# Kernel optimization log

Hardware: AMD Instinct MI355X
Metric: run time of the kernel (lower is better)

Reference implementation:

```python
import jax, jax.numpy as jnp
import numpy as np

DIM = 512
HEADS = 8
DIM_HEAD = 64
HIDDEN = HEADS * DIM_HEAD  # 512
B, H, W = 32, 64, 64


def setup_inputs() -> dict:
    key = jax.random.key(0)
    k1, k2, k3 = jax.random.split(key, 3)
    x = jax.random.normal(k1, (B, H, W, DIM), dtype=jnp.float32)
    w_qkv = jax.random.normal(k2, (DIM, 3 * HIDDEN), dtype=jnp.float32) * 0.02
    w_out = jax.random.normal(k3, (HIDDEN, DIM), dtype=jnp.float32) * 0.02
    b_out = jnp.zeros((DIM,), dtype=jnp.float32)
    return {"x": x, "w_qkv": w_qkv, "w_out": w_out, "b_out": b_out}


def reference(x, w_qkv, w_out, b_out):
    b, h, w, c = x.shape
    n = h * w
    scale = DIM_HEAD ** (-0.5)
    # 1x1 conv (no bias) == matmul over channels
    qkv = jnp.einsum('bhwc,cf->bhwf', x, w_qkv)  # (b, h, w, 3*hidden)
    q, k, v = jnp.split(qkv, 3, axis=-1)
    # 'b x y (h c) -> b (x y) h c'
    def to_heads(t):
        return t.reshape(b, n, HEADS, DIM_HEAD)
    q, k, v = map(to_heads, (q, k, v))
    q = q * scale
    # contraction over spatial axis d=(x*y): sim (b, dim_head_i, heads, dim_head_j)
    sim = jnp.einsum('bdhi,bdhj->bihj', q, k)
    sim = sim - jnp.max(sim, axis=-1, keepdims=True)
    attn = jax.nn.softmax(sim, axis=-1)
    out = jnp.einsum('bihj,bdhj->bdhi', attn, v)  # (b, n, heads, dim_head)
    out = out.reshape(b, h, w, HIDDEN)
    # output 1x1 conv with bias
    return jnp.einsum('bhwf,fc->bhwc', out, w_out) + b_out
```

## Files before the change

### kernel.cpp

```cpp
#include <hip/hip_runtime.h>
#include <hip/hip_bf16.h>
#include <stdint.h>

using bf16x8 = __attribute__((ext_vector_type(8))) __bf16;
using s16x8  = __attribute__((ext_vector_type(8))) short;
using f32x4  = __attribute__((ext_vector_type(4))) float;

__device__ __forceinline__ uint16_t f2bf(float f) {
    uint32_t u = __builtin_bit_cast(uint32_t, f);
    u += 0x7fffu + ((u >> 16) & 1u);
    return (uint16_t)(u >> 16);
}
__device__ __forceinline__ float bf2f(uint16_t h) {
    return __builtin_bit_cast(float, (uint32_t)h << 16);
}

__device__ __forceinline__ void async16(uint16_t* lds_dst, const uint16_t* g_src) {
    __builtin_amdgcn_global_load_lds(
        (const __attribute__((address_space(1))) void*)g_src,
        (__attribute__((address_space(3))) void*)lds_dst,
        16, 0, 0);
}

__global__ void wprep_all(const float* __restrict__ wqkv, const float* __restrict__ wout,
                          uint16_t* __restrict__ wqTs, uint16_t* __restrict__ wkTcat,
                          uint16_t* __restrict__ woutT, uint16_t* __restrict__ wv_rm)
{
    int sec = blockIdx.x >> 10;
    int idx = (blockIdx.x & 1023) * 256 + threadIdx.x;
    int co = idx >> 9, r = idx & 511;
    if (sec == 0) {
        wqTs[co * 512 + r] = f2bf(wqkv[r * 1536 + co] * 0.125f);
    } else if (sec == 1) {
        uint16_t v = f2bf(wqkv[r * 1536 + 512 + co]);
        wkTcat[co * 1024 + r] = v;
        wkTcat[co * 1024 + 512 + r] = v;
    } else if (sec == 2) {
        woutT[co * 512 + r] = f2bf(wout[r * 512 + co]);
    } else {
        wv_rm[co * 512 + r] = f2bf(wqkv[co * 1536 + 1024 + r]);
    }
}

__global__ __launch_bounds__(256, 4)
void xt_k(const float* __restrict__ x, uint16_t* __restrict__ xb, uint16_t* __restrict__ xT)
{
    __shared__ uint16_t lt[64 * 68];
    const int tid = threadIdx.x;
    const int bi = blockIdx.x;
    const int b = bi >> 9;
    const int rem = bi & 511;
    const int st = rem >> 3, ct = rem & 7;
    const int c4 = (tid & 15) * 4;
#pragma unroll
    for (int rep = 0; rep < 4; ++rep) {
        int r = (tid >> 4) + rep * 16;
        long gs = (long)(b * 4096 + st * 64 + r) * 512 + ct * 64 + c4;
        float4 v = *(const float4*)(x + gs);
        uint16_t t[4];
        t[0] = f2bf(v.x); t[1] = f2bf(v.y); t[2] = f2bf(v.z); t[3] = f2bf(v.w);
        *(ushort4*)(xb + gs) = *(const ushort4*)t;
#pragma unroll
        for (int q = 0; q < 4; ++q) lt[r * 68 + c4 + q] = t[q];
    }
    __syncthreads();
    const int s4 = (tid & 15) * 4;
#pragma unroll
    for (int rep = 0; rep < 4; ++rep) {
        int c = (tid >> 4) + rep * 16;
        uint16_t t[4];
#pragma unroll
        for (int q = 0; q < 4; ++q) t[q] = lt[(s4 + q) * 68 + c];
        *(ushort4*)(xT + (long)(b * 512 + ct * 64 + c) * 4096 + st * 64 + s4) =
            *(const ushort4*)t;
    }
}

template<bool OUTF32>
__global__ __launch_bounds__(512, 2)
void g8_k(const uint16_t* __restrict__ A, const uint16_t* __restrict__ Bt,
          void* __restrict__ Cp, const float* __restrict__ bias,
          int K, int lda, int ldb, int ldc, int mtiles, int ntiles,
          long abr, long bbe, long cbr)
{
    __shared__ uint16_t lds[65536];
    const int tid  = threadIdx.x;
    const int lane = tid & 63;
    const int wv   = tid >> 6;
    const int wr   = wv >> 2, wc = wv & 3;

    const int q8 = gridDim.x >> 3;
    const int l  = (blockIdx.x & 7) * q8 + (blockIdx.x >> 3);
    const int per   = mtiles * ntiles;
    const int batch = l / per;
    const int rem   = l - batch * per;
    const int mt    = rem / ntiles, nt = rem - mt * ntiles;

    const long arow0 = abr * batch + (long)mt * 256;
    const uint16_t* abase = A + arow0 * (long)lda;
    const uint16_t* btb   = Bt + bbe * batch + (long)nt * 256 * ldb;

    const int fr = lane & 15;
    const int cx0 = (((0 << 2) | (lane >> 4)) ^ (fr & 7)) * 8;
    const int cx1 = (((1 << 2) | (lane >> 4)) ^ (fr & 7)) * 8;
    const int baseA = wr * 8192 + fr * 64;
    const int baseB = (2 + (wc >> 1)) * 8192 + ((wc & 1) * 64 + fr) * 64;

    const int NT = K >> 6;

    auto stage = [&](int slot, const uint16_t* gb, int rstride, int k0) {
#pragma unroll
        for (int i = 0; i < 2; ++i) {
            int si = i * 512 + wv * 64 + lane;
            int rr = si >> 3, cc = (si & 7) ^ (rr & 7);
            async16(&lds[slot * 8192 + (i * 512 + wv * 64) * 8],
                    gb + (long)rr * rstride + k0 + cc * 8);
        }
    };

    f32x4 acc[8][4];
#pragma unroll
    for (int m = 0; m < 8; ++m)
#pragma unroll
        for (int n = 0; n < 4; ++n) acc[m][n] = (f32x4){0.f, 0.f, 0.f, 0.f};

    bf16x8 af[4], bfq[4];

    auto rdA = [&](int mb, int b4, int cx) {
#pragma unroll
        for (int mi = 0; mi < 4; ++mi)
            af[mi] = __builtin_bit_cast(bf16x8,
                *(const s16x8*)&lds[b4 * 8192 + baseA + (mb + mi) * 1024 + cx]);
    };
    auto rdB = [&](int b4, int cx) {
#pragma unroll
        for (int n = 0; n < 4; ++n)
            bfq[n] = __builtin_bit_cast(bf16x8,
                *(const s16x8*)&lds[b4 * 8192 + baseB + n * 1024 + cx]);
    };
    auto mm = [&](int mb) {
        asm volatile("s_waitcnt lgkmcnt(0)" ::: "memory");
        __builtin_amdgcn_sched_barrier(0);
        __builtin_amdgcn_s_setprio(1);
#pragma unroll
        for (int mi = 0; mi < 4; ++mi)
#pragma unroll
            for (int n = 0; n < 4; ++n)
                acc[mb + mi][n] = __builtin_amdgcn_mfma_f32_16x16x32_bf16(
                    af[mi], bfq[n], acc[mb + mi][n], 0, 0, 0);
        __builtin_amdgcn_s_setprio(0);
        __builtin_amdgcn_s_barrier();
    };

    stage(0, abase,              lda, 0);
    stage(1, abase + 128L * lda, lda, 0);
    stage(2, btb,                ldb, 0);
    stage(3, btb + 128L * ldb,   ldb, 0);
    stage(6, btb,                ldb, 64);
    stage(7, btb + 128L * ldb,   ldb, 64);
    asm volatile("s_waitcnt vmcnt(4)" ::: "memory");
    __builtin_amdgcn_sched_barrier(0);
    __builtin_amdgcn_s_barrier();

    for (int it = 0; it < (NT >> 1); ++it) {
        const int E = 2 * it, Od = E + 1;
        const bool s3 = (E + 2) < NT;
        const bool s7 = (Od + 2) < NT;
        const int kE2 = (E + 2) << 6, kO1 = Od << 6, kO2 = (Od + 2) << 6;

        rdB(0, cx0); rdA(0, 0, cx0);
        stage(4, abase,              lda, kO1);
        stage(5, abase + 128L * lda, lda, kO1);
        __builtin_amdgcn_s_barrier();
        mm(0);
        rdA(4, 0, cx0);
        __builtin_amdgcn_s_barrier();
        mm(4);
        rdB(0, cx1); rdA(0, 0, cx1);
        __builtin_amdgcn_s_barrier();
        mm(0);
        rdA(4, 0, cx1);
        if (s3) {
            stage(2, btb,              ldb, kE2);
            stage(3, btb + 128L * ldb, ldb, kE2);
            asm volatile("s_waitcnt vmcnt(4)" ::: "memory");
        } else {
            asm volatile("s_waitcnt vmcnt(0)" ::: "memory");
        }
        __builtin_amdgcn_sched_barrier(0);
        __builtin_amdgcn_s_barrier();
        mm(4);
        rdB(4, cx0); rdA(0, 4, cx0);
        if (s3) {
            stage(0, abase,              lda, kE2);
            stage(1, abase + 128L * lda, lda, kE2);
        }
        __builtin_amdgcn_s_barrier();
        mm(0);
        rdA(4, 4, cx0);
        __builtin_amdgcn_s_barrier();
        mm(4);
        rdB(4, cx1); rdA(0, 4, cx1);
        __builtin_amdgcn_s_barrier();
        mm(0);
        rdA(4, 4, cx1);
        if (s7) {
            stage(6, btb,              ldb, kO2);
            stage(7, btb + 128L * ldb, ldb, kO2);
            asm volatile("s_waitcnt vmcnt(4)" ::: "memory");
        } else {
            asm volatile("s_waitcnt vmcnt(0)" ::: "memory");
        }
        __builtin_amdgcn_sched_barrier(0);
        __builtin_amdgcn_s_barrier();
        mm(4);
    }

    const long crow0 = cbr * batch + (long)mt * 256 + wr * 128;
    const int  col0  = nt * 256 + wc * 64;
    float bv[4];
#pragma unroll
    for (int n = 0; n < 4; ++n)
        bv[n] = bias ? bias[col0 + n * 16 + (lane & 15)] : 0.f;
#pragma unroll
    for (int m = 0; m < 8; ++m) {
#pragma unroll
        for (int r = 0; r < 4; ++r) {
            long row = crow0 + m * 16 + (lane >> 4) * 4 + r;
#pragma unroll
            for (int n = 0; n < 4; ++n) {
                int col = col0 + n * 16 + (lane & 15);
                float v = acc[m][n][r];
                if constexpr (OUTF32)
                    ((float*)Cp)[row * (long)ldc + col] = v + bv[n];
                else
                    ((uint16_t*)Cp)[row * (long)ldc + col] = f2bf(v);
            }
        }
    }
}

__global__ __launch_bounds__(512, 2)
void g8G_k(const uint16_t* __restrict__ X, uint16_t* __restrict__ Gcat)
{
    __shared__ uint16_t lds[65536];
    const int tid  = threadIdx.x;
    const int lane = tid & 63;
    const int wv   = tid >> 6;
    const int wr   = wv >> 2, wc = wv & 3;

    const int q8 = gridDim.x >> 3;
    const int l  = (blockIdx.x & 7) * q8 + (blockIdx.x >> 3);
    const int g  = l / 3;
    const int quad = l - g * 3;
    const int b = g >> 1, z = g & 1;
    const int mt = (quad == 1) ? 1 : 0;
    const int nt = (quad == 0) ? 0 : 1;

    const uint16_t* xb0 = X + (long)b * 512 * 4096 + z * 2048;
    const uint16_t* abase = xb0 + (long)mt * 256 * 4096;
    const uint16_t* btb   = xb0 + (long)nt * 256 * 4096;

    const int fr = lane & 15;
    const int cx0 = (((0 << 2) | (lane >> 4)) ^ (fr & 7)) * 8;
    const int cx1 = (((1 << 2) | (lane >> 4)) ^ (fr & 7)) * 8;
    const int baseA = wr * 8192 + fr * 64;
    const int baseB = (2 + (wc >> 1)) * 8192 + ((wc & 1) * 64 + fr) * 64;

    const int NT = 32;

    auto stage = [&](int slot, const uint16_t* gb, int k0) {
#pragma unroll
        for (int i = 0; i < 2; ++i) {
            int si = i * 512 + wv * 64 + lane;
            int rr = si >> 3, cc = (si & 7) ^ (rr & 7);
            async16(&lds[slot * 8192 + (i * 512 + wv * 64) * 8],
                    gb + (long)rr * 4096 + k0 + cc * 8);
        }
    };

    f32x4 acc[8][4];
#pragma unroll
    for (int m = 0; m < 8; ++m)
#pragma unroll
        for (int n = 0; n < 4; ++n) acc[m][n] = (f32x4){0.f, 0.f, 0.f, 0.f};

    bf16x8 af[4], bfq[4];
    auto rdA = [&](int mb, int b4, int cx) {
#pragma unroll
        for (int mi = 0; mi < 4; ++mi)
            af[mi] = __builtin_bit_cast(bf16x8,
                *(const s16x8*)&lds[b4 * 8192 + baseA + (mb + mi) * 1024 + cx]);
    };
    auto rdB = [&](int b4, int cx) {
#pragma unroll
        for (int n = 0; n < 4; ++n)
            bfq[n] = __builtin_bit_cast(bf16x8,
                *(const s16x8*)&lds[b4 * 8192 + baseB + n * 1024 + cx]);
    };
    auto mm = [&](int mb) {
        asm volatile("s_waitcnt lgkmcnt(0)" ::: "memory");
        __builtin_amdgcn_sched_barrier(0);
        __builtin_amdgcn_s_setprio(1);
#pragma unroll
        for (int mi = 0; mi < 4; ++mi)
#pragma unroll
            for (int n = 0; n < 4; ++n)
                acc[mb + mi][n] = __builtin_amdgcn_mfma_f32_16x16x32_bf16(
                    af[mi], bfq[n], acc[mb + mi][n], 0, 0, 0);
        __builtin_amdgcn_s_setprio(0);
        __builtin_amdgcn_s_barrier();
    };

    stage(0, abase,               0);
    stage(1, abase + 128L * 4096, 0);
    stage(2, btb,                 0);
    stage(3, btb + 128L * 4096,   0);
    stage(6, btb,                 64);
    stage(7, btb + 128L * 4096,   64);
    asm volatile("s_waitcnt vmcnt(4)" ::: "memory");
    __builtin_amdgcn_sched_barrier(0);
    __builtin_amdgcn_s_barrier();

    for (int it = 0; it < (NT >> 1); ++it) {
        const int E = 2 * it, Od = E + 1;
        const bool s3 = (E + 2) < NT;
        const bool s7 = (Od + 2) < NT;
        const int kE2 = (E + 2) << 6, kO1 = Od << 6, kO2 = (Od + 2) << 6;

        rdB(0, cx0); rdA(0, 0, cx0);
        stage(4, abase,               kO1);
        stage(5, abase + 128L * 4096, kO1);
        __builtin_amdgcn_s_barrier();
        mm(0);
        rdA(4, 0, cx0);
        __builtin_amdgcn_s_barrier();
        mm(4);
        rdB(0, cx1); rdA(0, 0, cx1);
        __builtin_amdgcn_s_barrier();
        mm(0);
        rdA(4, 0, cx1);
        if (s3) {
            stage(2, btb,               kE2);
            stage(3, btb + 128L * 4096, kE2);
            asm volatile("s_waitcnt vmcnt(4)" ::: "memory");
        } else {
            asm volatile("s_waitcnt vmcnt(0)" ::: "memory");
        }
        __builtin_amdgcn_sched_barrier(0);
        __builtin_amdgcn_s_barrier();
        mm(4);
        rdB(4, cx0); rdA(0, 4, cx0);
        if (s3) {
            stage(0, abase,               kE2);
            stage(1, abase + 128L * 4096, kE2);
        }
        __builtin_amdgcn_s_barrier();
        mm(0);
        rdA(4, 4, cx0);
        __builtin_amdgcn_s_barrier();
        mm(4);
        rdB(4, cx1); rdA(0, 4, cx1);
        __builtin_amdgcn_s_barrier();
        mm(0);
        rdA(4, 4, cx1);
        if (s7) {
            stage(6, btb,               kO2);
            stage(7, btb + 128L * 4096, kO2);
            asm volatile("s_waitcnt vmcnt(4)" ::: "memory");
        } else {
            asm volatile("s_waitcnt vmcnt(0)" ::: "memory");
        }
        __builtin_amdgcn_sched_barrier(0);
        __builtin_amdgcn_s_barrier();
        mm(4);
    }

    uint16_t* o = Gcat + (long)b * 524288;
    const int zoff = z * 512;
    const int row0 = mt * 256 + wr * 128;
    const int col0 = nt * 256 + wc * 64;
#pragma unroll
    for (int m = 0; m < 8; ++m) {
#pragma unroll
        for (int r = 0; r < 4; ++r) {
            int row = row0 + m * 16 + (lane >> 4) * 4 + r;
#pragma unroll
            for (int n = 0; n < 4; ++n)
                o[(long)row * 1024 + zoff + col0 + n * 16 + (lane & 15)] = f2bf(acc[m][n][r]);
        }
        if (quad == 2) {
            int rbase = row0 + m * 16 + (lane >> 4) * 4;
#pragma unroll
            for (int n = 0; n < 4; ++n) {
                int col = col0 + n * 16 + (lane & 15);
                uint16_t t[4];
#pragma unroll
                for (int r = 0; r < 4; ++r) t[r] = f2bf(acc[m][n][r]);
                *(ushort4*)&o[(long)col * 1024 + zoff + rbase] = *(const ushort4*)t;
            }
        }
    }
}

__global__ __launch_bounds__(512, 1)
void simfull_k(const uint16_t* __restrict__ Gcat, const uint16_t* __restrict__ wkTcat,
               const uint16_t* __restrict__ wqTs, uint16_t* __restrict__ attnT)
{
    __shared__ uint16_t sm[73728];
    const int tid  = threadIdx.x;
    const int lane = tid & 63;
    const int wv   = tid >> 6;
    const int fr   = lane & 15;
    const int bi = blockIdx.x;
    const int h = bi >> 5;
    const int b = (bi & 7) * 4 + ((bi >> 3) & 3);

    const uint16_t* gb  = Gcat + (long)b * 524288;
    const uint16_t* ab  = wkTcat + (long)h * 64 * 1024;
    const uint16_t* qb2 = wqTs + (long)h * 64 * 512;

    f32x4 acc[4][4];
#pragma unroll
    for (int mf = 0; mf < 4; ++mf)
#pragma unroll
        for (int nf = 0; nf < 4; ++nf) acc[mf][nf] = (f32x4){0.f, 0.f, 0.f, 0.f};

    for (int t = 0; t < 16; ++t) {
        const int k0 = t * 64;
#pragma unroll
        for (int i = 0; i < 8; ++i) {
            int si = i * 64 + lane;
            int rr = si >> 3, cc = (si & 7) ^ (rr & 7);
            async16(&sm[wv * 4096 + i * 512],
                    gb + (long)(wv * 64 + rr) * 1024 + k0 + cc * 8);
        }
        {
            int rr = wv * 8 + (lane >> 3);
            int cc = (lane & 7) ^ (rr & 7);
            async16(&sm[32768 + wv * 512],
                    ab + (long)rr * 1024 + k0 + cc * 8);
        }
        asm volatile("s_waitcnt vmcnt(0)" ::: "memory");
        __syncthreads();
#pragma unroll
        for (int ks = 0; ks < 2; ++ks) {
            bf16x8 af[4], bfq[4];
            int cx = ((ks * 4 + (lane >> 4)) ^ (fr & 7)) * 8;
#pragma unroll
            for (int mf = 0; mf < 4; ++mf)
                af[mf] = __builtin_bit_cast(bf16x8,
                    *(const s16x8*)&sm[32768 + (mf * 16 + fr) * 64 + cx]);
#pragma unroll
            for (int nf = 0; nf < 4; ++nf)
                bfq[nf] = __builtin_bit_cast(bf16x8,
                    *(const s16x8*)&sm[(wv * 64 + nf * 16 + fr) * 64 + cx]);
#pragma unroll
            for (int mf = 0; mf < 4; ++mf)
#pragma unroll
                for (int nf = 0; nf < 4; ++nf)
                    acc[mf][nf] = __builtin_amdgcn_mfma_f32_16x16x32_bf16(
                        af[mf], bfq[nf], acc[mf][nf], 0, 0, 0);
        }
        __syncthreads();
    }

#pragma unroll
    for (int mf = 0; mf < 4; ++mf)
#pragma unroll
        for (int nf = 0; nf < 4; ++nf)
#pragma unroll
            for (int r = 0; r < 4; ++r) {
                int j = mf * 16 + (lane >> 4) * 4 + r;
                int c = wv * 64 + nf * 16 + fr;
                float v = acc[mf][nf][r];
                uint16_t hi = f2bf(v);
                int off = j * 512 + ((c >> 3) ^ (j & 7)) * 8 + (c & 7);
                sm[off] = hi;
                sm[32768 + off] = f2bf(v - bf2f(hi));
            }
    __syncthreads();

    f32x4 a2[4][4];
#pragma unroll
    for (int mf = 0; mf < 4; ++mf)
#pragma unroll
        for (int nf = 0; nf < 4; ++nf) a2[mf][nf] = (f32x4){0.f, 0.f, 0.f, 0.f};
#pragma unroll
    for (int ks = 0; ks < 2; ++ks) {
        bf16x8 af[4], bh[4], bl[4];
#pragma unroll
        for (int mf = 0; mf < 4; ++mf)
            af[mf] = __builtin_bit_cast(bf16x8,
                *(const s16x8*)&qb2[(long)(mf * 16 + fr) * 512 + wv * 64 + ks * 32 + (lane >> 4) * 8]);
#pragma unroll
        for (int nf = 0; nf < 4; ++nf) {
            int j = nf * 16 + fr;
            int ch = (wv * 8 + ks * 4 + (lane >> 4)) ^ (fr & 7);
            bh[nf] = __builtin_bit_cast(bf16x8, *(const s16x8*)&sm[j * 512 + ch * 8]);
            bl[nf] = __builtin_bit_cast(bf16x8, *(const s16x8*)&sm[32768 + j * 512 + ch * 8]);
        }
#pragma unroll
        for (int mf = 0; mf < 4; ++mf)
#pragma unroll
            for (int nf = 0; nf < 4; ++nf) {
                a2[mf][nf] = __builtin_amdgcn_mfma_f32_16x16x32_bf16(
                    af[mf], bh[nf], a2[mf][nf], 0, 0, 0);
                a2[mf][nf] = __builtin_amdgcn_mfma_f32_16x16x32_bf16(
                    af[mf], bl[nf], a2[mf][nf], 0, 0, 0);
            }
    }

    float* red = (float*)&sm[65536];
    for (int w = 0; w < 8; ++w) {
        if (wv == w) {
#pragma unroll
            for (int mf = 0; mf < 4; ++mf)
#pragma unroll
                for (int nf = 0; nf < 4; ++nf)
#pragma unroll
                    for (int r = 0; r < 4; ++r) {
                        int i = mf * 16 + (lane >> 4) * 4 + r;
                        int j = nf * 16 + fr;
                        float* p = &red[i * 64 + j];
                        *p = (w == 0) ? a2[mf][nf][r] : (*p + a2[mf][nf][r]);
                    }
        }
        __syncthreads();
    }

    float* rt1 = (float*)&sm[0];
    float* rt2 = (float*)&sm[512];
    const int i = tid >> 2, jc = tid & 3;
    float s[16];
    if (tid < 256) {
#pragma unroll
        for (int jj = 0; jj < 16; ++jj) s[jj] = red[i * 64 + jc * 16 + jj];
        float mx = s[0];
#pragma unroll
        for (int jj = 1; jj < 16; ++jj) mx = fmaxf(mx, s[jj]);
        rt1[i * 4 + jc] = mx;
    }
    __syncthreads();
    if (tid < 256) {
        float m4 = fmaxf(fmaxf(rt1[i * 4], rt1[i * 4 + 1]),
                         fmaxf(rt1[i * 4 + 2], rt1[i * 4 + 3]));
        float sum = 0.f;
#pragma unroll
        for (int jj = 0; jj < 16; ++jj) { s[jj] = __expf(s[jj] - m4); sum += s[jj]; }
        rt2[i * 4 + jc] = sum;
    }
    __syncthreads();
    if (tid < 256) {
        float tot = rt2[i * 4] + rt2[i * 4 + 1] + rt2[i * 4 + 2] + rt2[i * 4 + 3];
        float inv = 1.f / tot;
        uint16_t* at = attnT + (long)(b * 8 + h) * 4096;
#pragma unroll
        for (int jj = 0; jj < 16; ++jj)
            at[(jc * 16 + jj) * 64 + i] = f2bf(s[jj] * inv);
    }
}

__global__ __launch_bounds__(256, 1)
void w2_k(const uint16_t* __restrict__ attnT, const uint16_t* __restrict__ woutT,
          uint16_t* __restrict__ W2T)
{
    const int tid = threadIdx.x;
    const int lane = tid & 63, wv = tid >> 6;
    const int b = blockIdx.x >> 3, h = blockIdx.x & 7;
    const uint16_t* at = attnT + (long)blockIdx.x * 4096;

    bf16x8 bfrag[2][4];
#pragma unroll
    for (int ks = 0; ks < 2; ++ks)
#pragma unroll
        for (int nf = 0; nf < 4; ++nf) {
            s16x8 v = *(const s16x8*)&at[(nf * 16 + (lane & 15)) * 64 + ks * 32 + (lane >> 4) * 8];
            bfrag[ks][nf] = __builtin_bit_cast(bf16x8, v);
        }
    f32x4 acc[8][4];
#pragma unroll
    for (int mf = 0; mf < 8; ++mf)
#pragma unroll
        for (int nf = 0; nf < 4; ++nf) acc[mf][nf] = (f32x4){0.f, 0.f, 0.f, 0.f};
#pragma unroll
    for (int mf = 0; mf < 8; ++mf) {
        int c = wv * 128 + mf * 16 + (lane & 15);
#pragma unroll
        for (int ks = 0; ks < 2; ++ks) {
            s16x8 v = *(const s16x8*)&woutT[(long)c * 512 + h * 64 + ks * 32 + (lane >> 4) * 8];
            bf16x8 af = __builtin_bit_cast(bf16x8, v);
#pragma unroll
            for (int nf = 0; nf < 4; ++nf)
                acc[mf][nf] = __builtin_amdgcn_mfma_f32_16x16x32_bf16(
                    af, bfrag[ks][nf], acc[mf][nf], 0, 0, 0);
        }
    }
    uint16_t* o = W2T + (long)b * 512 * 512;
#pragma unroll
    for (int mf = 0; mf < 8; ++mf)
#pragma unroll
        for (int nf = 0; nf < 4; ++nf)
#pragma unroll
            for (int r = 0; r < 4; ++r) {
                int c = wv * 128 + mf * 16 + (lane >> 4) * 4 + r;
                int j = nf * 16 + (lane & 15);
                o[(long)c * 512 + h * 64 + j] = f2bf(acc[mf][nf][r]);
            }
}

extern "C" void kernel_launch(void* const* d_in, const int* in_sizes, int n_in,
                              void* d_out, int out_size, void* d_ws, size_t ws_size,
                              hipStream_t stream)
{
    const float* x     = (const float*)d_in[0];
    const float* w_qkv = (const float*)d_in[1];
    const float* w_out = (const float*)d_in[2];
    const float* b_out = (const float*)d_in[3];
    float* out = (float*)d_out;

    char* ws = (char*)d_ws;
    uint16_t* xb     = (uint16_t*)(ws);
    uint16_t* xT     = (uint16_t*)(ws + 134217728L);
    uint16_t* Gcat   = (uint16_t*)(ws + 268435456L);
    uint16_t* attnT  = (uint16_t*)(ws + 301989888L);
    uint16_t* W2T    = (uint16_t*)(ws + 304087040L);
    uint16_t* Bteff  = (uint16_t*)(ws + 320864256L);
    uint16_t* wqTs   = (uint16_t*)(ws + 354418688L);
    uint16_t* wkTcat = (uint16_t*)(ws + 354942976L);
    uint16_t* woutT  = (uint16_t*)(ws + 355991552L);
    uint16_t* wv_rm  = (uint16_t*)(ws + 356515840L);

    wprep_all<<<4096, 256, 0, stream>>>(w_qkv, w_out, wqTs, wkTcat, woutT, wv_rm);

    xt_k<<<16384, 256, 0, stream>>>(x, xb, xT);

    g8G_k<<<192, 512, 0, stream>>>(xT, Gcat);

    simfull_k<<<256, 512, 0, stream>>>(Gcat, wkTcat, wqTs, attnT);

    w2_k<<<256, 256, 0, stream>>>(attnT, woutT, W2T);

    g8_k<false><<<128, 512, 0, stream>>>(
        W2T, wv_rm, Bteff, nullptr,
        512, 512, 512, 512, 2, 2, 512L, 0L, 512L);

    g8_k<true><<<1024, 512, 0, stream>>>(
        xb, Bteff, out, b_out,
        512, 512, 512, 512, 16, 2, 4096L, 262144L, 4096L);
}
```

Before: 378.8 us.

## Fuse weight prep into transpose, pipeline simfull loads, fuse W2 and Wv GEMMs

The weight-prep kernel is merged into the x transpose/convert kernel as extra blocks, saving one launch. simfull_k's K loop now uses a three-stage async LDS ring with smaller k-steps, partial vmcnt waits and raised wave priority around the MFMAs, so global loads overlap with compute. The separate w2_k and g8_k<false> kernels are replaced by one w2v_k that, per head, computes attn·Wv into LDS and then accumulates Wout·(that) directly into Bteff. This removes the W2T intermediate and one launch, at the cost of recomputing the small per-head product in every block and a different order of bf16 rounding.

```diff
diff --git a/kernel.cpp b/kernel.cpp
--- a/kernel.cpp
+++ b/kernel.cpp
@@ -22,32 +22,33 @@
         16, 0, 0);
 }
 
-__global__ void wprep_all(const float* __restrict__ wqkv, const float* __restrict__ wout,
-                          uint16_t* __restrict__ wqTs, uint16_t* __restrict__ wkTcat,
-                          uint16_t* __restrict__ woutT, uint16_t* __restrict__ wv_rm)
-{
-    int sec = blockIdx.x >> 10;
-    int idx = (blockIdx.x & 1023) * 256 + threadIdx.x;
-    int co = idx >> 9, r = idx & 511;
-    if (sec == 0) {
-        wqTs[co * 512 + r] = f2bf(wqkv[r * 1536 + co] * 0.125f);
-    } else if (sec == 1) {
-        uint16_t v = f2bf(wqkv[r * 1536 + 512 + co]);
-        wkTcat[co * 1024 + r] = v;
-        wkTcat[co * 1024 + 512 + r] = v;
-    } else if (sec == 2) {
-        woutT[co * 512 + r] = f2bf(wout[r * 512 + co]);
-    } else {
-        wv_rm[co * 512 + r] = f2bf(wqkv[co * 1536 + 1024 + r]);
-    }
-}
-
 __global__ __launch_bounds__(256, 4)
-void xt_k(const float* __restrict__ x, uint16_t* __restrict__ xb, uint16_t* __restrict__ xT)
+void xtw_k(const float* __restrict__ x, const float* __restrict__ wqkv,
+           const float* __restrict__ wout,
+           uint16_t* __restrict__ xb, uint16_t* __restrict__ xT,
+           uint16_t* __restrict__ wqTs, uint16_t* __restrict__ wkTcat,
+           uint16_t* __restrict__ woutT, uint16_t* __restrict__ wv_rm)
 {
     __shared__ uint16_t lt[64 * 68];
     const int tid = threadIdx.x;
     const int bi = blockIdx.x;
+    if (bi >= 16384) {
+        int sec = (bi - 16384) >> 10;
+        int idx = ((bi - 16384) & 1023) * 256 + tid;
+        int co = idx >> 9, r = idx & 511;
+        if (sec == 0) {
+            wqTs[co * 512 + r] = f2bf(wqkv[r * 1536 + co] * 0.125f);
+        } else if (sec == 1) {
+            uint16_t v = f2bf(wqkv[r * 1536 + 512 + co]);
+            wkTcat[co * 1024 + r] = v;
+            wkTcat[co * 1024 + 512 + r] = v;
+        } else if (sec == 2) {
+            woutT[co * 512 + r] = f2bf(wout[r * 512 + co]);
+        } else {
+            wv_rm[co * 512 + r] = f2bf(wqkv[co * 1536 + 1024 + r]);
+        }
+        return;
+    }
     const int b = bi >> 9;
     const int rem = bi & 511;
     const int st = rem >> 3, ct = rem & 7;
@@ -405,13 +406,14 @@
 
 __global__ __launch_bounds__(512, 1)
 void simfull_k(const uint16_t* __restrict__ Gcat, const uint16_t* __restrict__ wkTcat,
-               const uint16_t* __restrict__ wqTs, uint16_t* __restrict__ attnT)
+               const uint16_t* __restrict__ wqTs, uint16_t* __restrict__ attn)
 {
     __shared__ uint16_t sm[73728];
     const int tid  = threadIdx.x;
     const int lane = tid & 63;
     const int wv   = tid >> 6;
     const int fr   = lane & 15;
+    const int hi4  = lane >> 4;
     const int bi = blockIdx.x;
     const int h = bi >> 5;
     const int b = (bi & 7) * 4 + ((bi >> 3) & 3);
@@ -420,49 +422,64 @@
     const uint16_t* ab  = wkTcat + (long)h * 64 * 1024;
     const uint16_t* qb2 = wqTs + (long)h * 64 * 512;
 
+    auto stg = [&](int q, int t) {
+        const int k0 = t * 32;
+#pragma unroll
+        for (int i = 0; i < 4; ++i) {
+            int si = i * 64 + lane;
+            int rr = si >> 2, cc = (si & 3) ^ ((rr >> 1) & 3);
+            async16(&sm[q * 16384 + wv * 2048 + i * 512],
+                    gb + (long)(wv * 64 + rr) * 1024 + k0 + cc * 8);
+        }
+        {
+            int si = (wv & 3) * 64 + lane;
+            int rr = si >> 2, cc = (si & 3) ^ ((rr >> 1) & 3);
+            async16(&sm[49152 + q * 4096 + (wv >> 2) * 2048 + (wv & 3) * 512],
+                    ab + (long)rr * 1024 + k0 + cc * 8);
+        }
+    };
+
     f32x4 acc[4][4];
 #pragma unroll
     for (int mf = 0; mf < 4; ++mf)
 #pragma unroll
         for (int nf = 0; nf < 4; ++nf) acc[mf][nf] = (f32x4){0.f, 0.f, 0.f, 0.f};
 
-    for (int t = 0; t < 16; ++t) {
-        const int k0 = t * 64;
-#pragma unroll
-        for (int i = 0; i < 8; ++i) {
-            int si = i * 64 + lane;
-            int rr = si >> 3, cc = (si & 7) ^ (rr & 7);
-            async16(&sm[wv * 4096 + i * 512],
-                    gb + (long)(wv * 64 + rr) * 1024 + k0 + cc * 8);
-        }
-        {
-            int rr = wv * 8 + (lane >> 3);
-            int cc = (lane & 7) ^ (rr & 7);
-            async16(&sm[32768 + wv * 512],
-                    ab + (long)rr * 1024 + k0 + cc * 8);
-        }
-        asm volatile("s_waitcnt vmcnt(0)" ::: "memory");
-        __syncthreads();
-#pragma unroll
-        for (int ks = 0; ks < 2; ++ks) {
-            bf16x8 af[4], bfq[4];
-            int cx = ((ks * 4 + (lane >> 4)) ^ (fr & 7)) * 8;
-#pragma unroll
-            for (int mf = 0; mf < 4; ++mf)
-                af[mf] = __builtin_bit_cast(bf16x8,
-                    *(const s16x8*)&sm[32768 + (mf * 16 + fr) * 64 + cx]);
+    const int sa = (hi4 ^ ((fr >> 1) & 3)) * 8;
+
+    stg(0, 0);
+    stg(1, 1);
+    asm volatile("s_waitcnt vmcnt(5)" ::: "memory");
+    __builtin_amdgcn_sched_barrier(0);
+    __builtin_amdgcn_s_barrier();
+
+    for (int t = 0; t < 32; ++t) {
+        const int q = t % 3;
+        if (t + 2 < 32) stg((t + 2) % 3, t + 2);
+        bf16x8 af[4], bfq[4];
+        const int wkb = 49152 + q * 4096 + (wv >> 2) * 2048;
+#pragma unroll
+        for (int mf = 0; mf < 4; ++mf)
+            af[mf] = __builtin_bit_cast(bf16x8,
+                *(const s16x8*)&sm[wkb + (mf * 16 + fr) * 32 + sa]);
+#pragma unroll
+        for (int nf = 0; nf < 4; ++nf)
+            bfq[nf] = __builtin_bit_cast(bf16x8,
+                *(const s16x8*)&sm[q * 16384 + wv * 2048 + (nf * 16 + fr) * 32 + sa]);
+        asm volatile("s_waitcnt lgkmcnt(0)" ::: "memory");
+        __builtin_amdgcn_sched_barrier(0);
+        __builtin_amdgcn_s_setprio(1);
+#pragma unroll
+        for (int mf = 0; mf < 4; ++mf)
 #pragma unroll
             for (int nf = 0; nf < 4; ++nf)
-                bfq[nf] = __builtin_bit_cast(bf16x8,
-                    *(const s16x8*)&sm[(wv * 64 + nf * 16 + fr) * 64 + cx]);
-#pragma unroll
-            for (int mf = 0; mf < 4; ++mf)
-#pragma unroll
-                for (int nf = 0; nf < 4; ++nf)
-                    acc[mf][nf] = __builtin_amdgcn_mfma_f32_16x16x32_bf16(
-                        af[mf], bfq[nf], acc[mf][nf], 0, 0, 0);
-        }
-        __syncthreads();
+                acc[mf][nf] = __builtin_amdgcn_mfma_f32_16x16x32_bf16(
+                    af[mf], bfq[nf], acc[mf][nf], 0, 0, 0);
+        __builtin_amdgcn_s_setprio(0);
+        if (t + 2 < 32) { asm volatile("s_waitcnt vmcnt(5)" ::: "memory"); }
+        else            { asm volatile("s_waitcnt vmcnt(0)" ::: "memory"); }
+        __builtin_amdgcn_sched_barrier(0);
+        __builtin_amdgcn_s_barrier();
     }
 
 #pragma unroll
@@ -471,7 +488,7 @@
         for (int nf = 0; nf < 4; ++nf)
 #pragma unroll
             for (int r = 0; r < 4; ++r) {
-                int j = mf * 16 + (lane >> 4) * 4 + r;
+                int j = mf * 16 + hi4 * 4 + r;
                 int c = wv * 64 + nf * 16 + fr;
                 float v = acc[mf][nf][r];
                 uint16_t hi = f2bf(v);
@@ -492,11 +509,11 @@
 #pragma unroll
         for (int mf = 0; mf < 4; ++mf)
             af[mf] = __builtin_bit_cast(bf16x8,
-                *(const s16x8*)&qb2[(long)(mf * 16 + fr) * 512 + wv * 64 + ks * 32 + (lane >> 4) * 8]);
+                *(const s16x8*)&qb2[(long)(mf * 16 + fr) * 512 + wv * 64 + ks * 32 + hi4 * 8]);
 #pragma unroll
         for (int nf = 0; nf < 4; ++nf) {
             int j = nf * 16 + fr;
-            int ch = (wv * 8 + ks * 4 + (lane >> 4)) ^ (fr & 7);
+            int ch = (wv * 8 + ks * 4 + hi4) ^ (fr & 7);
             bh[nf] = __builtin_bit_cast(bf16x8, *(const s16x8*)&sm[j * 512 + ch * 8]);
             bl[nf] = __builtin_bit_cast(bf16x8, *(const s16x8*)&sm[32768 + j * 512 + ch * 8]);
         }
@@ -520,7 +537,7 @@
                 for (int nf = 0; nf < 4; ++nf)
 #pragma unroll
                     for (int r = 0; r < 4; ++r) {
-                        int i = mf * 16 + (lane >> 4) * 4 + r;
+                        int i = mf * 16 + hi4 * 4 + r;
                         int j = nf * 16 + fr;
                         float* p = &red[i * 64 + j];
                         *p = (w == 0) ? a2[mf][nf][r] : (*p + a2[mf][nf][r]);
@@ -554,59 +571,111 @@
     if (tid < 256) {
         float tot = rt2[i * 4] + rt2[i * 4 + 1] + rt2[i * 4 + 2] + rt2[i * 4 + 3];
         float inv = 1.f / tot;
-        uint16_t* at = attnT + (long)(b * 8 + h) * 4096;
+        uint16_t* at = attn + (long)(b * 8 + h) * 4096;
 #pragma unroll
         for (int jj = 0; jj < 16; ++jj)
-            at[(jc * 16 + jj) * 64 + i] = f2bf(s[jj] * inv);
-    }
-}
-
-__global__ __launch_bounds__(256, 1)
-void w2_k(const uint16_t* __restrict__ attnT, const uint16_t* __restrict__ woutT,
-          uint16_t* __restrict__ W2T)
+            at[i * 64 + jc * 16 + jj] = f2bf(s[jj] * inv);
+    }
+}
+
+__global__ __launch_bounds__(512, 1)
+void w2v_k(const uint16_t* __restrict__ attn, const uint16_t* __restrict__ woutT,
+           const uint16_t* __restrict__ wv_rm, uint16_t* __restrict__ Bteff)
 {
-    const int tid = threadIdx.x;
-    const int lane = tid & 63, wv = tid >> 6;
-    const int b = blockIdx.x >> 3, h = blockIdx.x & 7;
-    const uint16_t* at = attnT + (long)blockIdx.x * 4096;
-
-    bf16x8 bfrag[2][4];
-#pragma unroll
-    for (int ks = 0; ks < 2; ++ks)
-#pragma unroll
-        for (int nf = 0; nf < 4; ++nf) {
-            s16x8 v = *(const s16x8*)&at[(nf * 16 + (lane & 15)) * 64 + ks * 32 + (lane >> 4) * 8];
-            bfrag[ks][nf] = __builtin_bit_cast(bf16x8, v);
-        }
+    __shared__ uint16_t RT[16384];
+    const int tid  = threadIdx.x;
+    const int lane = tid & 63;
+    const int wv8  = tid >> 6;
+    const int wr   = wv8 >> 2, wc = wv8 & 3;
+    const int fr   = lane & 15;
+    const int hi4  = lane >> 4;
+
+    const int q8 = gridDim.x >> 3;
+    const int l  = (blockIdx.x & 7) * q8 + (blockIdx.x >> 3);
+    const int b  = l >> 2;
+    const int mt = (l >> 1) & 1, nt = l & 1;
+
     f32x4 acc[8][4];
 #pragma unroll
+    for (int m = 0; m < 8; ++m)
+#pragma unroll
+        for (int n = 0; n < 4; ++n) acc[m][n] = (f32x4){0.f, 0.f, 0.f, 0.f};
+
+    for (int h = 0; h < 8; ++h) {
+        const uint16_t* ah = attn + (long)(b * 8 + h) * 4096;
+        f32x4 rac[4][2];
+#pragma unroll
+        for (int mf = 0; mf < 4; ++mf)
+#pragma unroll
+            for (int nf = 0; nf < 2; ++nf) rac[mf][nf] = (f32x4){0.f, 0.f, 0.f, 0.f};
+#pragma unroll
+        for (int ks = 0; ks < 2; ++ks) {
+            bf16x8 af[4], bf2[2];
+#pragma unroll
+            for (int mf = 0; mf < 4; ++mf)
+                af[mf] = __builtin_bit_cast(bf16x8,
+                    *(const s16x8*)&ah[(mf * 16 + fr) * 64 + ks * 32 + hi4 * 8]);
+#pragma unroll
+            for (int nf = 0; nf < 2; ++nf) {
+                int k = nt * 256 + wv8 * 32 + nf * 16 + fr;
+                bf2[nf] = __builtin_bit_cast(bf16x8,
+                    *(const s16x8*)&wv_rm[(long)k * 512 + h * 64 + ks * 32 + hi4 * 8]);
+            }
+#pragma unroll
+            for (int mf = 0; mf < 4; ++mf)
+#pragma unroll
+                for (int nf = 0; nf < 2; ++nf)
+                    rac[mf][nf] = __builtin_amdgcn_mfma_f32_16x16x32_bf16(
+                        af[mf], bf2[nf], rac[mf][nf], 0, 0, 0);
+        }
+        __syncthreads();
+#pragma unroll
+        for (int mf = 0; mf < 4; ++mf)
+#pragma unroll
+            for (int nf = 0; nf < 2; ++nf)
+#pragma unroll
+                for (int r = 0; r < 4; ++r) {
+                    int i2 = mf * 16 + hi4 * 4 + r;
+                    int k  = wv8 * 32 + nf * 16 + fr;
+                    RT[k * 64 + (((i2 >> 3) ^ (k & 7)) * 8) + (i2 & 7)] = f2bf(rac[mf][nf][r]);
+                }
+        __syncthreads();
+#pragma unroll
+        for (int ks = 0; ks < 2; ++ks) {
+            bf16x8 am[8], bm[4];
+#pragma unroll
+            for (int mf = 0; mf < 8; ++mf) {
+                int c = mt * 256 + wr * 128 + mf * 16 + fr;
+                am[mf] = __builtin_bit_cast(bf16x8,
+                    *(const s16x8*)&woutT[(long)c * 512 + h * 64 + ks * 32 + hi4 * 8]);
+            }
+#pragma unroll
+            for (int nf = 0; nf < 4; ++nf) {
+                int k = wc * 64 + nf * 16 + fr;
+                bm[nf] = __builtin_bit_cast(bf16x8,
+                    *(const s16x8*)&RT[k * 64 + (((ks * 4 + hi4) ^ (k & 7)) * 8)]);
+            }
+#pragma unroll
+            for (int mf = 0; mf < 8; ++mf)
+#pragma unroll
+                for (int nf = 0; nf < 4; ++nf)
+                    acc[mf][nf] = __builtin_amdgcn_mfma_f32_16x16x32_bf16(
+                        am[mf], bm[nf], acc[mf][nf], 0, 0, 0);
+        }
+    }
+
+    uint16_t* o = Bteff + (long)b * 262144;
+#pragma unroll
     for (int mf = 0; mf < 8; ++mf)
 #pragma unroll
-        for (int nf = 0; nf < 4; ++nf) acc[mf][nf] = (f32x4){0.f, 0.f, 0.f, 0.f};
-#pragma unroll
-    for (int mf = 0; mf < 8; ++mf) {
-        int c = wv * 128 + mf * 16 + (lane & 15);
-#pragma unroll
-        for (int ks = 0; ks < 2; ++ks) {
-            s16x8 v = *(const s16x8*)&woutT[(long)c * 512 + h * 64 + ks * 32 + (lane >> 4) * 8];
-            bf16x8 af = __builtin_bit_cast(bf16x8, v);
-#pragma unroll
-            for (int nf = 0; nf < 4; ++nf)
-                acc[mf][nf] = __builtin_amdgcn_mfma_f32_16x16x32_bf16(
-                    af, bfrag[ks][nf], acc[mf][nf], 0, 0, 0);
-        }
-    }
-    uint16_t* o = W2T + (long)b * 512 * 512;
-#pragma unroll
-    for (int mf = 0; mf < 8; ++mf)
-#pragma unroll
-        for (int nf = 0; nf < 4; ++nf)
-#pragma unroll
-            for (int r = 0; r < 4; ++r) {
-                int c = wv * 128 + mf * 16 + (lane >> 4) * 4 + r;
-                int j = nf * 16 + (lane & 15);
-                o[(long)c * 512 + h * 64 + j] = f2bf(acc[mf][nf][r]);
+        for (int r = 0; r < 4; ++r) {
+            int c = mt * 256 + wr * 128 + mf * 16 + hi4 * 4 + r;
+#pragma unroll
+            for (int nf = 0; nf < 4; ++nf) {
+                int k = nt * 256 + wc * 64 + nf * 16 + fr;
+                o[(long)c * 512 + k] = f2bf(acc[mf][nf][r]);
             }
+        }
 }
 
 extern "C" void kernel_launch(void* const* d_in, const int* in_sizes, int n_in,
@@ -623,27 +692,21 @@
     uint16_t* xb     = (uint16_t*)(ws);
     uint16_t* xT     = (uint16_t*)(ws + 134217728L);
     uint16_t* Gcat   = (uint16_t*)(ws + 268435456L);
-    uint16_t* attnT  = (uint16_t*)(ws + 301989888L);
-    uint16_t* W2T    = (uint16_t*)(ws + 304087040L);
+    uint16_t* attn   = (uint16_t*)(ws + 301989888L);
     uint16_t* Bteff  = (uint16_t*)(ws + 320864256L);
     uint16_t* wqTs   = (uint16_t*)(ws + 354418688L);
     uint16_t* wkTcat = (uint16_t*)(ws + 354942976L);
     uint16_t* woutT  = (uint16_t*)(ws + 355991552L);
     uint16_t* wv_rm  = (uint16_t*)(ws + 356515840L);
 
-    wprep_all<<<4096, 256, 0, stream>>>(w_qkv, w_out, wqTs, wkTcat, woutT, wv_rm);
-
-    xt_k<<<16384, 256, 0, stream>>>(x, xb, xT);
+    xtw_k<<<20480, 256, 0, stream>>>(x, w_qkv, w_out, xb, xT,
+                                     wqTs, wkTcat, woutT, wv_rm);
 
     g8G_k<<<192, 512, 0, stream>>>(xT, Gcat);
 
-    simfull_k<<<256, 512, 0, stream>>>(Gcat, wkTcat, wqTs, attnT);
-
-    w2_k<<<256, 256, 0, stream>>>(attnT, woutT, W2T);
-
-    g8_k<false><<<128, 512, 0, stream>>>(
-        W2T, wv_rm, Bteff, nullptr,
-        512, 512, 512, 512, 2, 2, 512L, 0L, 512L);
+    simfull_k<<<256, 512, 0, stream>>>(Gcat, wkTcat, wqTs, attn);
+
+    w2v_k<<<128, 512, 0, stream>>>(attn, woutT, wv_rm, Bteff);
 
     g8_k<true><<<1024, 512, 0, stream>>>(
         xb, Bteff, out, b_out,
```

Measured after the change: 393.0 us. +3.8%, slower.
